# Kernel tuning notes

Measured on AMD Instinct MI355X. Metric: run time of the kernel, lower is better.

## Reference

```python
import jax, jax.numpy as jnp
import numpy as np

D_MODEL = 2048
N_HEADS = 16
D_HEAD = D_MODEL // N_HEADS


def setup_inputs() -> dict:
    key = jax.random.key(0)
    k1, k2, k3, k4, k5 = jax.random.split(key, 5)
    x = jax.random.normal(k1, (4, 2048, D_MODEL), dtype=jnp.float32)
    s = 1.0 / np.sqrt(D_MODEL)
    qkv_w = jax.random.normal(k2, (3 * D_MODEL, D_MODEL), dtype=jnp.float32) * s
    qkv_b = jax.random.normal(k3, (3 * D_MODEL,), dtype=jnp.float32) * 0.01
    out_w = jax.random.normal(k4, (D_MODEL, D_MODEL), dtype=jnp.float32) * s
    out_b = jax.random.normal(k5, (D_MODEL,), dtype=jnp.float32) * 0.01
    return {"x": x, "qkv_w": qkv_w, "qkv_b": qkv_b, "out_w": out_w, "out_b": out_b}


def reference(x, qkv_w, qkv_b, out_w, out_b):
    B, T, D = x.shape
    # fused QKV projection: (B,T,D) -> (B,T,3D), torch Linear uses W^T
    qkv = jnp.einsum('btd,ed->bte', x, qkv_w) + qkv_b
    qkv = qkv.reshape(B, T, 3, N_HEADS, D_HEAD)
    qkv = jnp.transpose(qkv, (2, 0, 3, 1, 4))  # (3, B, H, T, Dh)
    q, k, v = qkv[0], qkv[1], qkv[2]
    # scaled dot-product attention (non-causal)
    scale = 1.0 / jnp.sqrt(jnp.asarray(D_HEAD, dtype=x.dtype))
    scores = jnp.einsum('bhqd,bhkd->bhqk', q, k) * scale
    attn = jax.nn.softmax(scores, axis=-1)
    out = jnp.einsum('bhqk,bhkd->bhqd', attn, v)
    out = jnp.transpose(out, (0, 2, 1, 3)).reshape(B, T, D)
    return jnp.einsum('btd,ed->bte', out, out_w) + out_b
```

## Files before the change

kernel.cpp:

```cpp
#include <hip/hip_runtime.h>

typedef unsigned short u16;
typedef __attribute__((ext_vector_type(8))) __bf16 bf16x8;
typedef __attribute__((ext_vector_type(4))) float f32x4;

#define SEQ 2048
#define DMODEL 2048
#define NHEADS 16
#define DHEAD 128

typedef __attribute__((address_space(1))) void gvoid_t;
typedef __attribute__((address_space(3))) void lvoid_t;

__device__ inline void gload_lds16(const void* g, void* l) {
  __builtin_amdgcn_global_load_lds((gvoid_t*)g, (lvoid_t*)l, 16, 0, 0);
}

__device__ inline u16 f2bf(float f) {
  unsigned u = __float_as_uint(f);
  unsigned r = (u + 0x7fffu + ((u >> 16) & 1u)) >> 16;
  return (u16)r;
}

__global__ __launch_bounds__(256) void cvt_f32_bf16(const float* __restrict__ in,
                                                    u16* __restrict__ out, int n4) {
  int i = blockIdx.x * 256 + threadIdx.x;
  if (i >= n4) return;
  float4 v = reinterpret_cast<const float4*>(in)[i];
  ushort4 o;
  o.x = f2bf(v.x); o.y = f2bf(v.y); o.z = f2bf(v.z); o.w = f2bf(v.w);
  reinterpret_cast<ushort4*>(out)[i] = o;
}

#define GBAR() __builtin_amdgcn_s_barrier()
#define SB0() __builtin_amdgcn_sched_barrier(0)
#define WAITLGKM(N) do { asm volatile("s_waitcnt lgkmcnt(" #N ")" ::: "memory"); } while (0)
#define WAITVM(N) do { asm volatile("s_waitcnt vmcnt(" #N ")" ::: "memory"); } while (0)

template <int MODE>
__global__ __launch_bounds__(512, 1) void gemm256(
    const u16* __restrict__ A, const u16* __restrict__ B,
    const float* __restrict__ bias, int M, int N, int K, int nby,
    u16* __restrict__ qb, u16* __restrict__ kb, u16* __restrict__ vtb,
    float* __restrict__ outf) {
  __shared__ __align__(16) u16 As[2][256 * 64];
  __shared__ __align__(16) u16 Bs[2][256 * 64];
  const int nwg = gridDim.x;
  const int cpx = nwg >> 3;
  const int bid = blockIdx.x;
  const int sw = (bid & 7) * cpx + (bid >> 3);
  const int bx = sw / nby, by = sw % nby;
  const int m0 = bx * 256, n0 = by * 256;
  const int tid = threadIdx.x, lane = tid & 63, w = tid >> 6;
  const int wm = w >> 2, wn = w & 3;
  const int fr = lane & 15, hi = lane >> 4;
  const int g4 = hi * 4;
  const u16* Abase = A + (size_t)m0 * K;
  const u16* Bbase = B + (size_t)n0 * K;

  f32x4 acc[8][4];
#pragma unroll
  for (int i = 0; i < 8; i++)
#pragma unroll
    for (int j = 0; j < 4; j++) acc[i][j] = f32x4{0.f, 0.f, 0.f, 0.f};

#define STAGE_A1(T, P, J)                                                        \
  do {                                                                           \
    const int U = ((J) * 8 + w) * 64 + lane;                                     \
    const int r_ = U >> 3;                                                       \
    const int us = (lane & 7) ^ (r_ & 7);                                        \
    gload_lds16(Abase + (size_t)r_ * K + (T) * 64 + us * 8, &As[P][U * 8]);      \
  } while (0)
#define STAGE_B1(T, P, J)                                                        \
  do {                                                                           \
    const int U = ((J) * 8 + w) * 64 + lane;                                     \
    const int r_ = U >> 3;                                                       \
    const int us = (lane & 7) ^ (r_ & 7);                                        \
    gload_lds16(Bbase + (size_t)r_ * K + (T) * 64 + us * 8, &Bs[P][U * 8]);      \
  } while (0)

#define LDA(AF, H, P)                                                            \
  do {                                                                           \
    _Pragma("unroll") for (int fi = 0; fi < 4; fi++) {                           \
      const int row = wm * 128 + (H) * 64 + fi * 16 + fr;                        \
      _Pragma("unroll") for (int kk = 0; kk < 2; kk++) {                         \
        const int u = (kk * 4 + hi) ^ (row & 7);                                 \
        AF[fi][kk] = *(const bf16x8*)&As[P][row * 64 + u * 8];                    \
      }                                                                          \
    }                                                                            \
  } while (0)

#define LDB(BF, G, P)                                                            \
  do {                                                                           \
    _Pragma("unroll") for (int fj = 0; fj < 2; fj++) {                           \
      const int row = wn * 64 + (G) * 32 + fj * 16 + fr;                         \
      _Pragma("unroll") for (int kk = 0; kk < 2; kk++) {                         \
        const int u = (kk * 4 + hi) ^ (row & 7);                                 \
        BF[fj][kk] = *(const bf16x8*)&Bs[P][row * 64 + u * 8];                    \
      }                                                                          \
    }                                                                            \
  } while (0)

#define MF(AF, BF, H, G)                                                         \
  do {                                                                           \
    __builtin_amdgcn_s_setprio(1);                                               \
    _Pragma("unroll") for (int kk = 0; kk < 2; kk++)                             \
    _Pragma("unroll") for (int fi = 0; fi < 4; fi++)                             \
    _Pragma("unroll") for (int fj = 0; fj < 2; fj++)                             \
      acc[(H) * 4 + fi][(G) * 2 + fj] = __builtin_amdgcn_mfma_f32_16x16x32_bf16( \
          AF[fi][kk], BF[fj][kk], acc[(H) * 4 + fi][(G) * 2 + fj], 0, 0, 0);     \
    __builtin_amdgcn_s_setprio(0);                                               \
  } while (0)

#define TILE(T, P)                                                               \
  do {                                                                           \
                                                                        \
    LDA(a, 0, P); LDB(b0, 0, P); SB0();                                          \
    GBAR(); WAITLGKM(0); SB0();                                                  \
    MF(a, b0, 0, 0);                                                             \
    GBAR();                                                                      \
                                                                        \
    LDB(b1, 1, P); SB0();                                                        \
    if ((T) + 2 < NT) { STAGE_A1((T) + 2, P, 0); STAGE_A1((T) + 2, P, 2); }      \
    SB0();                                                                       \
    GBAR(); WAITLGKM(0); SB0();                                                  \
    MF(a, b1, 0, 1);                                                             \
    GBAR();                                                                      \
                                                                        \
    LDA(a, 1, P); SB0();                                                         \
    if ((T) + 2 < NT) { STAGE_B1((T) + 2, P, 0); STAGE_B1((T) + 2, P, 1); }      \
    SB0();                                                                       \
    GBAR(); WAITLGKM(0); SB0();                                                  \
    MF(a, b0, 1, 0);                                                             \
    GBAR();                                                                      \
                                                                        \
    if ((T) + 2 < NT) {                                                          \
      STAGE_A1((T) + 2, P, 1); STAGE_A1((T) + 2, P, 3);                          \
      STAGE_B1((T) + 2, P, 2); STAGE_B1((T) + 2, P, 3);                          \
    }                                                                            \
    SB0();                                                                       \
    MF(a, b1, 1, 1);                                                             \
    if ((T) + 2 < NT) { WAITVM(8); }                                             \
    else if ((T) + 1 < NT) { WAITVM(0); }                                        \
    SB0();                                                                       \
    GBAR();                                                                      \
  } while (0)

  const int NT = K >> 6;
#pragma unroll
  for (int j = 0; j < 4; j++) { STAGE_A1(0, 0, j); STAGE_B1(0, 0, j); }
#pragma unroll
  for (int j = 0; j < 4; j++) { STAGE_A1(1, 1, j); STAGE_B1(1, 1, j); }
  WAITVM(8); SB0();
  GBAR(); SB0();

  bf16x8 a[4][2], b0[2][2], b1[2][2];
  for (int t = 0; t + 1 < NT; t += 2) {
    TILE(t, 0);
    TILE(t + 1, 1);
  }

  if (MODE == 0) {
    const int which = n0 >> 11;
#pragma unroll
    for (int mi = 0; mi < 8; mi++) {
      const int trow = m0 + wm * 128 + mi * 16 + g4;
      const int b = trow >> 11;
      const int t = trow & 2047;
#pragma unroll
      for (int nj = 0; nj < 4; nj++) {
        const int col = n0 + wn * 64 + nj * 16 + fr;
        const int h = (col >> 7) & 15;
        const int dh = col & 127;
        const float bv = bias[col];
        if (which == 2) {
          ushort4 pk;
          pk.x = f2bf(acc[mi][nj][0] + bv);
          pk.y = f2bf(acc[mi][nj][1] + bv);
          pk.z = f2bf(acc[mi][nj][2] + bv);
          pk.w = f2bf(acc[mi][nj][3] + bv);
          *reinterpret_cast<ushort4*>(vtb + ((size_t)(b * NHEADS + h) * DHEAD + dh) * SEQ + t) = pk;
        } else {
          u16* dst = (which == 0) ? qb : kb;
          const float sc = (which == 0) ? 0.08838834764831845f : 1.0f;
#pragma unroll
          for (int r = 0; r < 4; r++)
            dst[((size_t)(b * NHEADS + h) * SEQ + (t + r)) * DHEAD + dh] =
                f2bf((acc[mi][nj][r] + bv) * sc);
        }
      }
    }
  } else {
#pragma unroll
    for (int mi = 0; mi < 8; mi++) {
      const int row = m0 + wm * 128 + mi * 16 + g4;
#pragma unroll
      for (int nj = 0; nj < 4; nj++) {
        const int col = n0 + wn * 64 + nj * 16 + fr;
        const float bv = bias[col];
#pragma unroll
        for (int r = 0; r < 4; r++) outf[(size_t)(row + r) * N + col] = acc[mi][nj][r] + bv;
      }
    }
  }
#undef STAGE_A1
#undef STAGE_B1
#undef LDA
#undef LDB
#undef MF
#undef TILE
}

__global__ __launch_bounds__(256, 2) void attn_fwd(const u16* __restrict__ Q,
                                                   const u16* __restrict__ Kb,
                                                   const u16* __restrict__ VT,
                                                   u16* __restrict__ O) {
  __shared__ __align__(16) u16 Ks[64 * 128];
  __shared__ __align__(16) u16 Vs[128 * 64];
  __shared__ __align__(16) u16 P_lds[4][32][72];
  const int bh = blockIdx.y;
  const int b = bh >> 4, h = bh & 15;
  const int w = threadIdx.x >> 6;
  const int lane = threadIdx.x & 63;
  const int fr = lane & 15;
  const int hi = lane >> 4;
  const int kr = hi * 8;
  const int g4 = hi * 4;
  const int q0w = blockIdx.x * 128 + w * 32;

  const u16* Qp = Q + (size_t)bh * SEQ * DHEAD;
  const u16* Kp = Kb + (size_t)bh * SEQ * DHEAD;
  const u16* Vp = VT + (size_t)bh * DHEAD * SEQ;

  bf16x8 qf[2][4];
#pragma unroll
  for (int mg = 0; mg < 2; mg++)
#pragma unroll
    for (int kk = 0; kk < 4; kk++)
      qf[mg][kk] = *(const bf16x8*)(Qp + (size_t)(q0w + mg * 16 + fr) * DHEAD + kk * 32 + kr);

  f32x4 oacc[2][8];
#pragma unroll
  for (int mg = 0; mg < 2; mg++)
#pragma unroll
    for (int i = 0; i < 8; i++) oacc[mg][i] = f32x4{0.f, 0.f, 0.f, 0.f};
  float mrun[2] = {-1e30f, -1e30f};
  float lrun[2] = {0.f, 0.f};

  bf16x8 kreg[4], vreg[4];
#pragma unroll
  for (int i = 0; i < 4; i++) {
    const int u = w * 256 + i * 64 + lane;
    const int rK = u >> 4, c16 = u & 15;
    kreg[i] = *(const bf16x8*)(Kp + (size_t)rK * DHEAD + c16 * 8);
    const int rV = u >> 3, c8 = u & 7;
    vreg[i] = *(const bf16x8*)(Vp + (size_t)rV * SEQ + c8 * 8);
  }

  for (int kv0 = 0; kv0 < SEQ; kv0 += 64) {
    __syncthreads();
#pragma unroll
    for (int i = 0; i < 4; i++) {
      const int u = w * 256 + i * 64 + lane;
      const int rK = u >> 4, c16 = u & 15;
      *(bf16x8*)&Ks[rK * 128 + ((c16 ^ (rK & 7)) * 8)] = kreg[i];
      const int rV = u >> 3, c8 = u & 7;
      *(bf16x8*)&Vs[rV * 64 + ((c8 ^ (rV & 7)) * 8)] = vreg[i];
    }
    __syncthreads();
    if (kv0 + 64 < SEQ) {
      const int kvn = kv0 + 64;
#pragma unroll
      for (int i = 0; i < 4; i++) {
        const int u = w * 256 + i * 64 + lane;
        const int rK = u >> 4, c16 = u & 15;
        kreg[i] = *(const bf16x8*)(Kp + (size_t)(kvn + rK) * DHEAD + c16 * 8);
        const int rV = u >> 3, c8 = u & 7;
        vreg[i] = *(const bf16x8*)(Vp + (size_t)rV * SEQ + kvn + c8 * 8);
      }
    }

    f32x4 s[2][4];
#pragma unroll
    for (int mg = 0; mg < 2; mg++)
#pragma unroll
      for (int ct = 0; ct < 4; ct++) s[mg][ct] = f32x4{0.f, 0.f, 0.f, 0.f};
    __builtin_amdgcn_s_setprio(1);
#pragma unroll
    for (int kk = 0; kk < 4; kk++) {
#pragma unroll
      for (int ct = 0; ct < 4; ct++) {
        const int row = ct * 16 + fr;
        bf16x8 kf = *(const bf16x8*)&Ks[row * 128 + (((kk * 4 + hi) ^ (row & 7)) * 8)];
        s[0][ct] = __builtin_amdgcn_mfma_f32_16x16x32_bf16(kf, qf[0][kk], s[0][ct], 0, 0, 0);
        s[1][ct] = __builtin_amdgcn_mfma_f32_16x16x32_bf16(kf, qf[1][kk], s[1][ct], 0, 0, 0);
      }
    }
    __builtin_amdgcn_s_setprio(0);

    float pm[2];
#pragma unroll
    for (int mg = 0; mg < 2; mg++) {
      f32x4 mv = s[mg][0];
      mv[0] = fmaxf(mv[0], s[mg][1][0]); mv[1] = fmaxf(mv[1], s[mg][1][1]);
      mv[2] = fmaxf(mv[2], s[mg][1][2]); mv[3] = fmaxf(mv[3], s[mg][1][3]);
      mv[0] = fmaxf(mv[0], s[mg][2][0]); mv[1] = fmaxf(mv[1], s[mg][2][1]);
      mv[2] = fmaxf(mv[2], s[mg][2][2]); mv[3] = fmaxf(mv[3], s[mg][2][3]);
      mv[0] = fmaxf(mv[0], s[mg][3][0]); mv[1] = fmaxf(mv[1], s[mg][3][1]);
      mv[2] = fmaxf(mv[2], s[mg][3][2]); mv[3] = fmaxf(mv[3], s[mg][3][3]);
      float p = fmaxf(fmaxf(mv[0], mv[1]), fmaxf(mv[2], mv[3]));
      p = fmaxf(p, __shfl_xor(p, 16, 64));
      p = fmaxf(p, __shfl_xor(p, 32, 64));
      pm[mg] = p;
    }

    const bool need = (pm[0] - mrun[0] > 8.f) || (pm[1] - mrun[1] > 8.f);
    if (__any(need)) {
#pragma unroll
      for (int mg = 0; mg < 2; mg++) {
        float nm = fmaxf(mrun[mg], pm[mg]);
        float sfv = __expf(mrun[mg] - nm);
        mrun[mg] = nm;
        lrun[mg] *= sfv;
        float fac[4];
#pragma unroll
        for (int r = 0; r < 4; r++) fac[r] = __shfl(sfv, g4 + r, 64);
#pragma unroll
        for (int dt = 0; dt < 8; dt++) {
          oacc[mg][dt][0] *= fac[0]; oacc[mg][dt][1] *= fac[1];
          oacc[mg][dt][2] *= fac[2]; oacc[mg][dt][3] *= fac[3];
        }
      }
    }

#pragma unroll
    for (int mg = 0; mg < 2; mg++) {
#pragma unroll
      for (int ct = 0; ct < 4; ct++)
#pragma unroll
        for (int r = 0; r < 4; r++) s[mg][ct][r] = __expf(s[mg][ct][r] - mrun[mg]);
      f32x4 sv = s[mg][0] + s[mg][1] + s[mg][2] + s[mg][3];
      float su = (sv[0] + sv[1]) + (sv[2] + sv[3]);
      su += __shfl_xor(su, 16, 64);
      su += __shfl_xor(su, 32, 64);
      lrun[mg] += su;
#pragma unroll
      for (int ct = 0; ct < 4; ct++) {
        ushort4 pk;
        pk.x = f2bf(s[mg][ct][0]); pk.y = f2bf(s[mg][ct][1]);
        pk.z = f2bf(s[mg][ct][2]); pk.w = f2bf(s[mg][ct][3]);
        *reinterpret_cast<ushort4*>(&P_lds[w][mg * 16 + fr][ct * 16 + g4]) = pk;
      }
    }

    bf16x8 pf[2][2];
#pragma unroll
    for (int mg = 0; mg < 2; mg++)
#pragma unroll
      for (int kk = 0; kk < 2; kk++)
        pf[mg][kk] = *(const bf16x8*)&P_lds[w][mg * 16 + fr][kk * 32 + kr];
    __builtin_amdgcn_s_setprio(1);
#pragma unroll
    for (int kk = 0; kk < 2; kk++) {
#pragma unroll
      for (int dt = 0; dt < 8; dt++) {
        const int row = dt * 16 + fr;
        bf16x8 vf = *(const bf16x8*)&Vs[row * 64 + (((kk * 4 + hi) ^ (row & 7)) * 8)];
        oacc[0][dt] = __builtin_amdgcn_mfma_f32_16x16x32_bf16(pf[0][kk], vf, oacc[0][dt], 0, 0, 0);
        oacc[1][dt] = __builtin_amdgcn_mfma_f32_16x16x32_bf16(pf[1][kk], vf, oacc[1][dt], 0, 0, 0);
      }
    }
    __builtin_amdgcn_s_setprio(0);
  }

#pragma unroll
  for (int mg = 0; mg < 2; mg++) {
    float linv = 1.0f / lrun[mg];
    float fac[4];
#pragma unroll
    for (int r = 0; r < 4; r++) fac[r] = __shfl(linv, g4 + r, 64);
#pragma unroll
    for (int r = 0; r < 4; r++) {
      const int t = q0w + mg * 16 + g4 + r;
      u16* op = O + ((size_t)(b * SEQ + t)) * DMODEL + h * DHEAD;
#pragma unroll
      for (int dt = 0; dt < 8; dt++) op[dt * 16 + fr] = f2bf(oacc[mg][dt][r] * fac[r]);
    }
  }
}

extern "C" void kernel_launch(void* const* d_in, const int* in_sizes, int n_in,
                              void* d_out, int out_size, void* d_ws, size_t ws_size,
                              hipStream_t stream) {
  const float* x = (const float*)d_in[0];
  const float* qkv_w = (const float*)d_in[1];
  const float* qkv_b = (const float*)d_in[2];
  const float* out_w = (const float*)d_in[3];
  const float* out_b = (const float*)d_in[4];
  float* out = (float*)d_out;

  char* ws = (char*)d_ws;
  u16* xb = (u16*)ws;
  u16* wqkv = (u16*)(ws + 33554432);
  u16* qb = (u16*)(ws + 33554432 + 25165824);
  u16* kb = qb + (size_t)64 * SEQ * DHEAD;
  u16* vtb = kb + (size_t)64 * SEQ * DHEAD;
  u16* attnb = xb;
  u16* outwb = wqkv;

  cvt_f32_bf16<<<16777216 / 4 / 256, 256, 0, stream>>>(x, xb, 16777216 / 4);
  cvt_f32_bf16<<<12582912 / 4 / 256, 256, 0, stream>>>(qkv_w, wqkv, 12582912 / 4);
  gemm256<0><<<768, 512, 0, stream>>>(xb, wqkv, qkv_b, 8192, 6144, 2048, 24, qb, kb, vtb,
                                      nullptr);
  cvt_f32_bf16<<<4194304 / 4 / 256, 256, 0, stream>>>(out_w, outwb, 4194304 / 4);
  dim3 ga(SEQ / 128, 64);
  attn_fwd<<<ga, 256, 0, stream>>>(qb, kb, vtb, attnb);
  gemm256<1><<<256, 512, 0, stream>>>(attnb, outwb, out_b, 8192, 2048, 2048, 8, nullptr,
                                      nullptr, nullptr, out);
}
```

Before: 479.7 us.

## Prefetch next tile's LDS fragments at end of GEMM tile and regroup stages

After: 491.9 us. 1.03x slower.

```diff
diff --git a/kernel.cpp b/kernel.cpp
--- a/kernel.cpp
+++ b/kernel.cpp
@@ -112,38 +112,39 @@
     __builtin_amdgcn_s_setprio(0);                                               \
   } while (0)
 
-#define TILE(T, P)                                                               \
+#define TILE(T, P, QB)                                                           \
   do {                                                                           \
                                                                         \
-    LDA(a, 0, P); LDB(b0, 0, P); SB0();                                          \
-    GBAR(); WAITLGKM(0); SB0();                                                  \
+    GBAR(); SB0();                                                               \
+    WAITLGKM(0); SB0();                                                          \
     MF(a, b0, 0, 0);                                                             \
-    GBAR();                                                                      \
+    GBAR(); SB0();                                                               \
                                                                         \
-    LDB(b1, 1, P); SB0();                                                        \
-    if ((T) + 2 < NT) { STAGE_A1((T) + 2, P, 0); STAGE_A1((T) + 2, P, 2); }      \
-    SB0();                                                                       \
-    GBAR(); WAITLGKM(0); SB0();                                                  \
+    if ((T) + 2 < NT) { STAGE_A1((T) + 2, P, 0); STAGE_A1((T) + 2, P, 2);        \
+                        STAGE_B1((T) + 2, P, 0); STAGE_B1((T) + 2, P, 1); }      \
+    SB0();                                                                       \
     MF(a, b1, 0, 1);                                                             \
-    GBAR();                                                                      \
+    SB0();                                                                       \
+    LDA(a, 1, P);                                                                \
+    SB0();                                                                       \
+    GBAR(); SB0();                                                               \
                                                                         \
-    LDA(a, 1, P); SB0();                                                         \
-    if ((T) + 2 < NT) { STAGE_B1((T) + 2, P, 0); STAGE_B1((T) + 2, P, 1); }      \
-    SB0();                                                                       \
-    GBAR(); WAITLGKM(0); SB0();                                                  \
+    if ((T) + 2 < NT) { STAGE_A1((T) + 2, P, 1); STAGE_A1((T) + 2, P, 3);        \
+                        STAGE_B1((T) + 2, P, 2); STAGE_B1((T) + 2, P, 3); }      \
+    SB0();                                                                       \
+    WAITLGKM(0); SB0();                                                          \
     MF(a, b0, 1, 0);                                                             \
-    GBAR();                                                                      \
+    GBAR(); SB0();                                                               \
                                                                         \
-    if ((T) + 2 < NT) {                                                          \
-      STAGE_A1((T) + 2, P, 1); STAGE_A1((T) + 2, P, 3);                          \
-      STAGE_B1((T) + 2, P, 2); STAGE_B1((T) + 2, P, 3);                          \
-    }                                                                            \
-    SB0();                                                                       \
     MF(a, b1, 1, 1);                                                             \
     if ((T) + 2 < NT) { WAITVM(8); }                                             \
     else if ((T) + 1 < NT) { WAITVM(0); }                                        \
     SB0();                                                                       \
-    GBAR();                                                                      \
+    GBAR(); SB0();                                                               \
+    if ((T) + 1 < NT) {                                                          \
+      LDA(a, 0, QB); LDB(b0, 0, QB); LDB(b1, 1, QB);                             \
+    }                                                                            \
+    SB0();                                                                       \
   } while (0)
 
   const int NT = K >> 6;
@@ -155,9 +156,11 @@
   GBAR(); SB0();
 
   bf16x8 a[4][2], b0[2][2], b1[2][2];
+  LDA(a, 0, 0); LDB(b0, 0, 0); LDB(b1, 1, 0);
+  SB0();
   for (int t = 0; t + 1 < NT; t += 2) {
-    TILE(t, 0);
-    TILE(t + 1, 1);
+    TILE(t, 0, 1);
+    TILE(t + 1, 1, 0);
   }
 
   if (MODE == 0) {
```
